# Kernel optimization log

Hardware: AMD Instinct MI355X
Metric: run time of the kernel (lower is better)

The kernel has to match this reference:

```python
import jax, jax.numpy as jnp
import numpy as np

INPUT_SIZE = 128
HIDDEN_SIZE = 128
OUTPUT_SIZE = 67  # hardcoded in the original module
SEQ_LEN = 512
BATCH = 2048


def setup_inputs() -> dict:
    key = jax.random.key(0)
    ks = jax.random.split(key, 7)
    x = jax.random.normal(ks[0], (INPUT_SIZE, SEQ_LEN, BATCH), dtype=jnp.float32)
    hidden = jax.random.normal(ks[1], (HIDDEN_SIZE, BATCH), dtype=jnp.float32)
    # bernoulli(0.5) mask applied column-wise to the initial hidden state
    drop_mask = jax.random.bernoulli(ks[2], 0.5, (HIDDEN_SIZE, BATCH)).astype(jnp.float32)
    # small init scale so tanh does not saturate
    Wi2h = jax.random.normal(ks[3], (HIDDEN_SIZE, INPUT_SIZE + HIDDEN_SIZE), dtype=jnp.float32) * 0.05
    bi2h = jax.random.normal(ks[4], (HIDDEN_SIZE,), dtype=jnp.float32) * 0.05
    Wi2o = jax.random.normal(ks[5], (OUTPUT_SIZE, HIDDEN_SIZE), dtype=jnp.float32) * 0.05
    bi2o = jax.random.normal(ks[6], (OUTPUT_SIZE,), dtype=jnp.float32) * 0.05
    return {"x": x, "hidden": hidden, "drop_mask": drop_mask,
            "Wi2h": Wi2h, "bi2h": bi2h, "Wi2o": Wi2o, "bi2o": bi2o}


def reference(x, hidden, drop_mask, Wi2h, bi2h, Wi2o, bi2o):
    # x: [input_size, seq_len, batch]; hidden: [hidden_size, batch]
    h0 = hidden * drop_mask  # per-column bernoulli dropout on initial state
    xs = jnp.transpose(x, (1, 0, 2))  # [seq, input_size, batch]

    def step(h, x_t):
        # combined = cat([x_t, h], dim=0).T -> [batch, input+hidden]
        combined = jnp.concatenate([x_t, h], axis=0).T
        h_new = jnp.tanh(combined @ Wi2h.T + bi2h)        # [batch, hidden]
        out = jax.nn.relu(h_new @ Wi2o.T + bi2o)          # [batch, output]
        return h_new.T, out.T                             # carry [hidden, batch], y [output, batch]

    _, ys = jax.lax.scan(step, h0, xs)  # ys: [seq, output, batch]
    Y = jnp.transpose(ys, (1, 0, 2))    # [output, seq, batch]
    return Y
```

## Files before the change

### kernel.cpp

```cpp
#include <hip/hip_runtime.h>
#include <hip/hip_bf16.h>
#include <stdint.h>

#define IN_SZ 128
#define HID 128
#define OUT_SZ 67
#define SEQ 512
#define BATCH 2048
#define BT 8
#define NTHR 512
#define SB (SEQ * BATCH)

typedef __attribute__((ext_vector_type(4))) float f32x4;
typedef __attribute__((ext_vector_type(8))) short s16x8;
typedef __attribute__((ext_vector_type(8))) __bf16 bf16x8;

static __device__ __forceinline__ unsigned short f2bf(float f) {
  union { float f; uint32_t u; } c; c.f = f;
  uint32_t u = c.u;
  uint32_t r = u + 0x7FFFu + ((u >> 16) & 1u);
  return (unsigned short)(r >> 16);
}
static __device__ __forceinline__ uint32_t pk2bf(float lo, float hi) {
  __hip_bfloat162 h2 = __float22bfloat162_rn(float2{lo, hi});
  union { __hip_bfloat162 h; uint32_t u; } c; c.h = h2;
  return c.u;
}
static __device__ __forceinline__ float fast_tanh(float x) {
  float e = __builtin_amdgcn_exp2f(x * 2.885390081777927f);
  float r = __builtin_amdgcn_rcpf(e + 1.f);
  return __builtin_fmaf(-2.f, r, 1.f);
}
static __device__ __forceinline__ void mfma16(f32x4& c, s16x8 a, s16x8 b) {
  c = __builtin_amdgcn_mfma_f32_16x16x32_bf16(
        __builtin_bit_cast(bf16x8, a), __builtin_bit_cast(bf16x8, b), c, 0, 0, 0);
}
#define KOFF(g, j) (4 * (g) + ((j) & 3) + (((j) >> 2) << 4))

static __device__ __forceinline__ void frag_barrier() {
  asm volatile("s_waitcnt lgkmcnt(0)");
  __builtin_amdgcn_s_barrier();
}

__global__ __launch_bounds__(NTHR, 1) void rnn_kernel(
    const float* __restrict__ x, const float* __restrict__ hidden,
    const float* __restrict__ mask, const float* __restrict__ Wi2h,
    const float* __restrict__ bi2h, const float* __restrict__ Wi2o,
    const float* __restrict__ bi2o, float* __restrict__ Y) {

  __shared__ s16x8 sF[2][8][64];

  const int tid = threadIdx.x;
  const int wave = tid >> 6;
  const int lane = tid & 63;
  const int g = lane >> 4;
  const int n16 = lane & 15;
  const int bid = ((blockIdx.x & 7) << 5) | (blockIdx.x >> 3);
  const int b0 = bid * BT;

  s16x8 W[8];
#pragma unroll
  for (int kt = 0; kt < 8; ++kt) {
    const float* wr = Wi2h + (size_t)(16 * wave + n16) * (IN_SZ + HID);
    s16x8 w8;
#pragma unroll
    for (int j = 0; j < 8; ++j)
      w8[j] = (short)f2bf(wr[32 * kt + KOFF(g, j)]);
    W[kt] = w8;
  }

  const bool hasO = (wave < 5);
  s16x8 wO[4];
#pragma unroll
  for (int kk = 0; kk < 4; ++kk) {
    s16x8 a;
#pragma unroll
    for (int j = 0; j < 8; ++j) {
      int m = 16 * wave + n16;
      a[j] = (short)((hasO && m < OUT_SZ)
                     ? f2bf(Wi2o[(size_t)m * HID + 32 * kk + KOFF(g, j)]) : 0);
    }
    wO[kk] = a;
  }

  f32x4 bhv, bov;
#pragma unroll
  for (int r = 0; r < 4; ++r) {
    bhv[r] = bi2h[16 * wave + 4 * g + r];
    int m = 16 * wave + 4 * g + r;
    bov[r] = (hasO && m < OUT_SZ) ? bi2o[m] : 0.f;
  }

  const int lc = tid & 7;
  const int lrb = tid >> 3;
  const int R0 = 2 * lrb;
  const int skk = R0 >> 5;
  const int r5 = R0 & 31;
  const int sg = (r5 < 16) ? (r5 >> 2) : ((r5 - 16) >> 2);
  const int sq = ((r5 & 2) >> 1) + ((r5 < 16) ? 0 : 2);
  const int slane = (sg << 4) | lc;
  const char* const xB = (const char*)x;
  uint32_t xrb[2];
#pragma unroll
  for (int i = 0; i < 2; ++i)
    xrb[i] = ((uint32_t)(R0 + i) * (uint32_t)SB + (uint32_t)(b0 + lc)) * 4u;

  {
    float v0 = *(const float*)(xB + xrb[0]);
    float v1 = *(const float*)(xB + xrb[1]);
    ((uint32_t*)&sF[0][skk][slane])[sq] = pk2bf(v0, v1);
    uint32_t h0o = (uint32_t)R0 * (uint32_t)BATCH + (uint32_t)(b0 + lc);
    uint32_t h1o = (uint32_t)(R0 + 1) * (uint32_t)BATCH + (uint32_t)(b0 + lc);
    float hv0 = hidden[(size_t)h0o] * mask[(size_t)h0o];
    float hv1 = hidden[(size_t)h1o] * mask[(size_t)h1o];
    ((uint32_t*)&sF[0][4 + skk][slane])[sq] = pk2bf(hv0, hv1);
  }
  float xq0[2], xq1[2], xq2[2], xq3[2];
#pragma unroll
  for (int i = 0; i < 2; ++i) {
    xq0[i] = *(const float*)(xB + xrb[i] + 1u * BATCH * 4u);
    xq1[i] = *(const float*)(xB + xrb[i] + 2u * BATCH * 4u);
    xq2[i] = *(const float*)(xB + xrb[i] + 3u * BATCH * 4u);
    xq3[i] = *(const float*)(xB + xrb[i] + 4u * BATCH * 4u);
  }
  frag_barrier();

  const uint32_t ybase = (uint32_t)(16 * wave + 4 * g) * (uint32_t)SB + (uint32_t)(b0 + n16);
  uint32_t* const hdst0 = (uint32_t*)&sF[0][4 + (wave >> 1)][lane] + (wave & 1) * 2;
  uint32_t* const hdst1 = (uint32_t*)&sF[1][4 + (wave >> 1)][lane] + (wave & 1) * 2;

#define STEP(T, P, XQ)                                                          \
  {                                                                             \
    const int t = (T);                                                          \
    const int pn = (P) ^ 1;                                                     \
                  \
    ((uint32_t*)&sF[pn][skk][slane])[sq] = pk2bf(XQ[0], XQ[1]);                 \
                                          \
    {                                                                           \
      const uint32_t tn = (uint32_t)((t + 5 > 511) ? 511 : t + 5) * (BATCH * 4u); \
      XQ[0] = *(const float*)(xB + xrb[0] + tn);                                \
      XQ[1] = *(const float*)(xB + xrb[1] + tn);                                \
    }                                                                           \
                                        \
    s16x8 X0 = sF[P][0][lane], X1 = sF[P][1][lane];                             \
    s16x8 X2 = sF[P][2][lane], X3 = sF[P][3][lane];                             \
    s16x8 H0 = sF[P][4][lane], H1 = sF[P][5][lane];                             \
    s16x8 H2 = sF[P][6][lane], H3 = sF[P][7][lane];                             \
                         \
    f32x4 a = bhv, a2 = {0.f, 0.f, 0.f, 0.f};                                   \
    mfma16(a, W[4], H0);  mfma16(a2, W[5], H1);                                 \
    mfma16(a, W[6], H2);  mfma16(a2, W[7], H3);                                 \
    mfma16(a, W[0], X0);  mfma16(a2, W[1], X1);                                 \
    mfma16(a, W[2], X2);  mfma16(a2, W[3], X3);                                 \
                                                   \
    if (hasO && t > 0) {                                                        \
      const uint32_t ty = (uint32_t)(t - 1) * (uint32_t)BATCH;                  \
      f32x4 ao = bov;                                                           \
      mfma16(ao, wO[0], H0); mfma16(ao, wO[1], H1);                             \
      mfma16(ao, wO[2], H2); mfma16(ao, wO[3], H3);                             \
      if (n16 < BT) {                                                           \
        _Pragma("unroll")                                                       \
        for (int r = 0; r < 4; ++r)                                             \
          if (16 * wave + 4 * g + r < OUT_SZ)                                   \
            Y[(size_t)(ybase + (uint32_t)r * SB + ty)] = fmaxf(ao[r], 0.f);     \
      }                                                                         \
    }                                                                           \
                      \
    {                                                                           \
      f32x4 s0 = a + a2;                                                        \
      uint32_t hp[2];                                                           \
      hp[0] = pk2bf(fast_tanh(s0[0]), fast_tanh(s0[1]));                        \
      hp[1] = pk2bf(fast_tanh(s0[2]), fast_tanh(s0[3]));                        \
      uint32_t* hd = pn ? hdst1 : hdst0;                                        \
      *(uint64_t*)hd = *(uint64_t*)hp;                                          \
    }                                                                           \
    frag_barrier();                                                             \
  }

  for (int t4 = 0; t4 < SEQ; t4 += 4) {
    STEP(t4 + 0, 0, xq0);
    STEP(t4 + 1, 1, xq1);
    STEP(t4 + 2, 0, xq2);
    STEP(t4 + 3, 1, xq3);
  }
#undef STEP

  if (hasO) {
    s16x8 H0 = sF[0][4][lane], H1 = sF[0][5][lane];
    s16x8 H2 = sF[0][6][lane], H3 = sF[0][7][lane];
    const uint32_t ty = 511u * (uint32_t)BATCH;
    f32x4 ao = bov;
    mfma16(ao, wO[0], H0); mfma16(ao, wO[1], H1);
    mfma16(ao, wO[2], H2); mfma16(ao, wO[3], H3);
    if (n16 < BT) {
#pragma unroll
      for (int r = 0; r < 4; ++r)
        if (16 * wave + 4 * g + r < OUT_SZ)
          Y[(size_t)(ybase + (uint32_t)r * SB + ty)] = fmaxf(ao[r], 0.f);
    }
  }
}

extern "C" void kernel_launch(void* const* d_in, const int* in_sizes, int n_in,
                              void* d_out, int out_size, void* d_ws, size_t ws_size,
                              hipStream_t stream) {
  const float* x      = (const float*)d_in[0];
  const float* hidden = (const float*)d_in[1];
  const float* mask   = (const float*)d_in[2];
  const float* Wi2h   = (const float*)d_in[3];
  const float* bi2h   = (const float*)d_in[4];
  const float* Wi2o   = (const float*)d_in[5];
  const float* bi2o   = (const float*)d_in[6];
  float* Y = (float*)d_out;
  (void)in_sizes; (void)n_in; (void)out_size; (void)d_ws; (void)ws_size;
  rnn_kernel<<<dim3(BATCH / BT), dim3(NTHR), 0, stream>>>(
      x, hidden, mask, Wi2h, bi2h, Wi2o, bi2o, Y);
}
```

Baseline: 530.5 us.

## Stage x via global_load_lds ring and move output MFMA off critical path

Replaces register-held prefetch of x with direct global-to-LDS DMA loads into a 4-slot ring buffer, so each step reads its x slice from LDS after a vmcnt wait. The tanh/h-write now happens before the barrier and the output projection with its Y stores is moved after the barrier, taking it off the recurrent critical path. The x-part MFMAs go into separate accumulators to shorten dependency chains. The risk is that the vmcnt(4) counting mixes with the Y stores' vmem counts, and ring-slot reuse timing may stall or race.

```diff
diff --git a/kernel.cpp b/kernel.cpp
--- a/kernel.cpp
+++ b/kernel.cpp
@@ -15,6 +15,9 @@
 typedef __attribute__((ext_vector_type(8))) short s16x8;
 typedef __attribute__((ext_vector_type(8))) __bf16 bf16x8;
 
+typedef const uint32_t __attribute__((address_space(1))) gu32_t;
+typedef uint32_t __attribute__((address_space(3))) su32_t;
+
 static __device__ __forceinline__ unsigned short f2bf(float f) {
   union { float f; uint32_t u; } c; c.f = f;
   uint32_t u = c.u;
@@ -41,6 +44,10 @@
   asm volatile("s_waitcnt lgkmcnt(0)");
   __builtin_amdgcn_s_barrier();
 }
+static __device__ __forceinline__ void dma4(const float* src, float* dst) {
+  __builtin_amdgcn_global_load_lds((gu32_t*)(const void*)src,
+                                   (su32_t*)(void*)dst, 4, 0, 0);
+}
 
 __global__ __launch_bounds__(NTHR, 1) void rnn_kernel(
     const float* __restrict__ x, const float* __restrict__ hidden,
@@ -49,6 +56,7 @@
     const float* __restrict__ bi2o, float* __restrict__ Y) {
 
   __shared__ s16x8 sF[2][8][64];
+  __shared__ float sX[4][1024];
 
   const int tid = threadIdx.x;
   const int wave = tid >> 6;
@@ -90,6 +98,9 @@
     int m = 16 * wave + 4 * g + r;
     bov[r] = (hasO && m < OUT_SZ) ? bi2o[m] : 0.f;
   }
+
+  const float* dma0 = x + (size_t)(16 * wave + (lane >> 3)) * SB + b0 + (lane & 7);
+  const float* dma1 = dma0 + (size_t)8 * SB;
 
   const int lc = tid & 7;
   const int lrb = tid >> 3;
@@ -99,15 +110,11 @@
   const int sg = (r5 < 16) ? (r5 >> 2) : ((r5 - 16) >> 2);
   const int sq = ((r5 & 2) >> 1) + ((r5 < 16) ? 0 : 2);
   const int slane = (sg << 4) | lc;
-  const char* const xB = (const char*)x;
-  uint32_t xrb[2];
-#pragma unroll
-  for (int i = 0; i < 2; ++i)
-    xrb[i] = ((uint32_t)(R0 + i) * (uint32_t)SB + (uint32_t)(b0 + lc)) * 4u;
+  const int e0 = R0 * 8 + lc;
 
   {
-    float v0 = *(const float*)(xB + xrb[0]);
-    float v1 = *(const float*)(xB + xrb[1]);
+    float v0 = x[(size_t)R0 * SB + b0 + lc];
+    float v1 = x[(size_t)(R0 + 1) * SB + b0 + lc];
     ((uint32_t*)&sF[0][skk][slane])[sq] = pk2bf(v0, v1);
     uint32_t h0o = (uint32_t)R0 * (uint32_t)BATCH + (uint32_t)(b0 + lc);
     uint32_t h1o = (uint32_t)(R0 + 1) * (uint32_t)BATCH + (uint32_t)(b0 + lc);
@@ -115,44 +122,59 @@
     float hv1 = hidden[(size_t)h1o] * mask[(size_t)h1o];
     ((uint32_t*)&sF[0][4 + skk][slane])[sq] = pk2bf(hv0, hv1);
   }
-  float xq0[2], xq1[2], xq2[2], xq3[2];
-#pragma unroll
-  for (int i = 0; i < 2; ++i) {
-    xq0[i] = *(const float*)(xB + xrb[i] + 1u * BATCH * 4u);
-    xq1[i] = *(const float*)(xB + xrb[i] + 2u * BATCH * 4u);
-    xq2[i] = *(const float*)(xB + xrb[i] + 3u * BATCH * 4u);
-    xq3[i] = *(const float*)(xB + xrb[i] + 4u * BATCH * 4u);
-  }
+
+#define STAGE(T, D)                                                             \
+  {                                                                             \
+    const uint32_t tp = ((T) > 511 ? 511u : (uint32_t)(T)) * (uint32_t)BATCH;   \
+    dma4(dma0 + tp, &sX[D][128 * wave]);                                        \
+    dma4(dma1 + tp, &sX[D][128 * wave + 64]);                                   \
+  }
+
+  STAGE(1, 1)
+  STAGE(2, 2)
+  STAGE(3, 3)
   frag_barrier();
 
   const uint32_t ybase = (uint32_t)(16 * wave + 4 * g) * (uint32_t)SB + (uint32_t)(b0 + n16);
   uint32_t* const hdst0 = (uint32_t*)&sF[0][4 + (wave >> 1)][lane] + (wave & 1) * 2;
   uint32_t* const hdst1 = (uint32_t*)&sF[1][4 + (wave >> 1)][lane] + (wave & 1) * 2;
 
-#define STEP(T, P, XQ)                                                          \
+#define STEP(T, P, D)                                                           \
   {                                                                             \
     const int t = (T);                                                          \
     const int pn = (P) ^ 1;                                                     \
-                  \
-    ((uint32_t*)&sF[pn][skk][slane])[sq] = pk2bf(XQ[0], XQ[1]);                 \
-                                          \
-    {                                                                           \
-      const uint32_t tn = (uint32_t)((t + 5 > 511) ? 511 : t + 5) * (BATCH * 4u); \
-      XQ[0] = *(const float*)(xB + xrb[0] + tn);                                \
-      XQ[1] = *(const float*)(xB + xrb[1] + tn);                                \
-    }                                                                           \
                                         \
     s16x8 X0 = sF[P][0][lane], X1 = sF[P][1][lane];                             \
     s16x8 X2 = sF[P][2][lane], X3 = sF[P][3][lane];                             \
     s16x8 H0 = sF[P][4][lane], H1 = sF[P][5][lane];                             \
     s16x8 H2 = sF[P][6][lane], H3 = sF[P][7][lane];                             \
-                         \
+                                   \
     f32x4 a = bhv, a2 = {0.f, 0.f, 0.f, 0.f};                                   \
-    mfma16(a, W[4], H0);  mfma16(a2, W[5], H1);                                 \
-    mfma16(a, W[6], H2);  mfma16(a2, W[7], H3);                                 \
-    mfma16(a, W[0], X0);  mfma16(a2, W[1], X1);                                 \
-    mfma16(a, W[2], X2);  mfma16(a2, W[3], X3);                                 \
-                                                   \
+    f32x4 ax = {0.f, 0.f, 0.f, 0.f}, ax2 = {0.f, 0.f, 0.f, 0.f};                \
+    mfma16(a, W[4], H0);   mfma16(a2, W[5], H1);                                \
+    mfma16(ax, W[0], X0);  mfma16(ax2, W[1], X1);                               \
+    mfma16(a, W[6], H2);   mfma16(a2, W[7], H3);                                \
+    mfma16(ax, W[2], X2);  mfma16(ax2, W[3], X3);                               \
+       \
+    {                                                                           \
+      f32x4 s0 = (a + a2) + (ax + ax2);                                         \
+      uint32_t hp[2];                                                           \
+      hp[0] = pk2bf(fast_tanh(s0[0]), fast_tanh(s0[1]));                        \
+      hp[1] = pk2bf(fast_tanh(s0[2]), fast_tanh(s0[3]));                        \
+      uint32_t* hd = pn ? hdst1 : hdst0;                                        \
+      *(uint64_t*)hd = *(uint64_t*)hp;                                          \
+    }                                                                           \
+                   \
+    asm volatile("s_waitcnt vmcnt(4)");                                         \
+    __builtin_amdgcn_sched_barrier(0);                                          \
+    {                                                                           \
+      float v0 = sX[D][e0];                                                     \
+      float v1 = sX[D][e0 + 8];                                                 \
+      ((uint32_t*)&sF[pn][skk][slane])[sq] = pk2bf(v0, v1);                     \
+    }                                                                           \
+                                                         \
+    frag_barrier();                                                             \
+              \
     if (hasO && t > 0) {                                                        \
       const uint32_t ty = (uint32_t)(t - 1) * (uint32_t)BATCH;                  \
       f32x4 ao = bov;                                                           \
@@ -165,25 +187,17 @@
             Y[(size_t)(ybase + (uint32_t)r * SB + ty)] = fmaxf(ao[r], 0.f);     \
       }                                                                         \
     }                                                                           \
-                      \
-    {                                                                           \
-      f32x4 s0 = a + a2;                                                        \
-      uint32_t hp[2];                                                           \
-      hp[0] = pk2bf(fast_tanh(s0[0]), fast_tanh(s0[1]));                        \
-      hp[1] = pk2bf(fast_tanh(s0[2]), fast_tanh(s0[3]));                        \
-      uint32_t* hd = pn ? hdst1 : hdst0;                                        \
-      *(uint64_t*)hd = *(uint64_t*)hp;                                          \
-    }                                                                           \
-    frag_barrier();                                                             \
+    STAGE(t + 4, (T) & 3)                                                       \
   }
 
   for (int t4 = 0; t4 < SEQ; t4 += 4) {
-    STEP(t4 + 0, 0, xq0);
-    STEP(t4 + 1, 1, xq1);
-    STEP(t4 + 2, 0, xq2);
-    STEP(t4 + 3, 1, xq3);
+    STEP(t4 + 0, 0, 1);
+    STEP(t4 + 1, 1, 2);
+    STEP(t4 + 2, 0, 3);
+    STEP(t4 + 3, 1, 0);
   }
 #undef STEP
+#undef STAGE
 
   if (hasO) {
     s16x8 H0 = sF[0][4][lane], H1 = sF[0][5][lane];
```

Result: slower. 673.9 us (+27.0%).

## Precompute next step's input projection off the recurrent critical path

Applied to the files above, without the earlier changes.

Splits the shared fragment buffer into separate hidden (double-buffered) and input (triple-buffered) arrays. The x-part MFMAs for step t+1 are issued during step t, so each step's dependent chain after the barrier is only the four hidden-state MFMAs plus tanh. The tanh and hidden write are also moved ahead of the output projection and Y stores. Sched barriers are added around the frag barrier to pin instruction ordering, which costs more registers and a 6-way unrolled loop with a tail.

```diff
diff --git a/kernel.cpp b/kernel.cpp
--- a/kernel.cpp
+++ b/kernel.cpp
@@ -38,8 +38,10 @@
 #define KOFF(g, j) (4 * (g) + ((j) & 3) + (((j) >> 2) << 4))
 
 static __device__ __forceinline__ void frag_barrier() {
+  __builtin_amdgcn_sched_barrier(0);
   asm volatile("s_waitcnt lgkmcnt(0)");
   __builtin_amdgcn_s_barrier();
+  __builtin_amdgcn_sched_barrier(0);
 }
 
 __global__ __launch_bounds__(NTHR, 1) void rnn_kernel(
@@ -48,7 +50,8 @@
     const float* __restrict__ bi2h, const float* __restrict__ Wi2o,
     const float* __restrict__ bi2o, float* __restrict__ Y) {
 
-  __shared__ s16x8 sF[2][8][64];
+  __shared__ s16x8 sH[2][4][64];
+  __shared__ s16x8 sX[3][4][64];
 
   const int tid = threadIdx.x;
   const int wave = tid >> 6;
@@ -100,94 +103,105 @@
   const int sq = ((r5 & 2) >> 1) + ((r5 < 16) ? 0 : 2);
   const int slane = (sg << 4) | lc;
   const char* const xB = (const char*)x;
-  uint32_t xrb[2];
-#pragma unroll
-  for (int i = 0; i < 2; ++i)
-    xrb[i] = ((uint32_t)(R0 + i) * (uint32_t)SB + (uint32_t)(b0 + lc)) * 4u;
+  const uint32_t xrb0 = ((uint32_t)R0 * (uint32_t)SB + (uint32_t)(b0 + lc)) * 4u;
+  const uint32_t xrb1 = ((uint32_t)(R0 + 1) * (uint32_t)SB + (uint32_t)(b0 + lc)) * 4u;
 
   {
-    float v0 = *(const float*)(xB + xrb[0]);
-    float v1 = *(const float*)(xB + xrb[1]);
-    ((uint32_t*)&sF[0][skk][slane])[sq] = pk2bf(v0, v1);
+    float v0 = *(const float*)(xB + xrb0);
+    float v1 = *(const float*)(xB + xrb1);
+    ((uint32_t*)&sX[0][skk][slane])[sq] = pk2bf(v0, v1);
+    float w0 = *(const float*)(xB + xrb0 + BATCH * 4u);
+    float w1 = *(const float*)(xB + xrb1 + BATCH * 4u);
+    ((uint32_t*)&sX[1][skk][slane])[sq] = pk2bf(w0, w1);
     uint32_t h0o = (uint32_t)R0 * (uint32_t)BATCH + (uint32_t)(b0 + lc);
     uint32_t h1o = (uint32_t)(R0 + 1) * (uint32_t)BATCH + (uint32_t)(b0 + lc);
     float hv0 = hidden[(size_t)h0o] * mask[(size_t)h0o];
     float hv1 = hidden[(size_t)h1o] * mask[(size_t)h1o];
-    ((uint32_t*)&sF[0][4 + skk][slane])[sq] = pk2bf(hv0, hv1);
-  }
-  float xq0[2], xq1[2], xq2[2], xq3[2];
-#pragma unroll
-  for (int i = 0; i < 2; ++i) {
-    xq0[i] = *(const float*)(xB + xrb[i] + 1u * BATCH * 4u);
-    xq1[i] = *(const float*)(xB + xrb[i] + 2u * BATCH * 4u);
-    xq2[i] = *(const float*)(xB + xrb[i] + 3u * BATCH * 4u);
-    xq3[i] = *(const float*)(xB + xrb[i] + 4u * BATCH * 4u);
-  }
+    ((uint32_t*)&sH[0][skk][slane])[sq] = pk2bf(hv0, hv1);
+  }
+  float xqA[2], xqB[2];
+  xqA[0] = *(const float*)(xB + xrb0 + 2u * BATCH * 4u);
+  xqA[1] = *(const float*)(xB + xrb1 + 2u * BATCH * 4u);
+  xqB[0] = *(const float*)(xB + xrb0 + 3u * BATCH * 4u);
+  xqB[1] = *(const float*)(xB + xrb1 + 3u * BATCH * 4u);
   frag_barrier();
 
   const uint32_t ybase = (uint32_t)(16 * wave + 4 * g) * (uint32_t)SB + (uint32_t)(b0 + n16);
-  uint32_t* const hdst0 = (uint32_t*)&sF[0][4 + (wave >> 1)][lane] + (wave & 1) * 2;
-  uint32_t* const hdst1 = (uint32_t*)&sF[1][4 + (wave >> 1)][lane] + (wave & 1) * 2;
-
-#define STEP(T, P, XQ)                                                          \
-  {                                                                             \
-    const int t = (T);                                                          \
-    const int pn = (P) ^ 1;                                                     \
-                  \
-    ((uint32_t*)&sF[pn][skk][slane])[sq] = pk2bf(XQ[0], XQ[1]);                 \
+  uint32_t* const hdst0 = (uint32_t*)&sH[0][wave >> 1][lane] + (wave & 1) * 2;
+  uint32_t* const hdst1 = (uint32_t*)&sH[1][wave >> 1][lane] + (wave & 1) * 2;
+
+  f32x4 axA = bhv, axA2 = {0.f, 0.f, 0.f, 0.f};
+  f32x4 axB, axB2;
+  {
+    s16x8 X0 = sX[0][0][lane], X1 = sX[0][1][lane];
+    s16x8 X2 = sX[0][2][lane], X3 = sX[0][3][lane];
+    mfma16(axA, W[0], X0);  mfma16(axA2, W[1], X1);
+    mfma16(axA, W[2], X2);  mfma16(axA2, W[3], X3);
+  }
+
+#define ITER(K, SR, SW, HPAR, XQ, AXI, AXI2, AXO, AXO2)                        \
+  {                                                                            \
+    const int t = t6 + (K);                                                    \
+    s16x8 H0 = sH[HPAR][0][lane], H1 = sH[HPAR][1][lane];                      \
+    s16x8 H2 = sH[HPAR][2][lane], H3 = sH[HPAR][3][lane];                      \
+    s16x8 Xn0 = sX[SR][0][lane], Xn1 = sX[SR][1][lane];                        \
+    s16x8 Xn2 = sX[SR][2][lane], Xn3 = sX[SR][3][lane];                        \
                                           \
-    {                                                                           \
-      const uint32_t tn = (uint32_t)((t + 5 > 511) ? 511 : t + 5) * (BATCH * 4u); \
-      XQ[0] = *(const float*)(xB + xrb[0] + tn);                                \
-      XQ[1] = *(const float*)(xB + xrb[1] + tn);                                \
-    }                                                                           \
-                                        \
-    s16x8 X0 = sF[P][0][lane], X1 = sF[P][1][lane];                             \
-    s16x8 X2 = sF[P][2][lane], X3 = sF[P][3][lane];                             \
-    s16x8 H0 = sF[P][4][lane], H1 = sF[P][5][lane];                             \
-    s16x8 H2 = sF[P][6][lane], H3 = sF[P][7][lane];                             \
-                         \
-    f32x4 a = bhv, a2 = {0.f, 0.f, 0.f, 0.f};                                   \
-    mfma16(a, W[4], H0);  mfma16(a2, W[5], H1);                                 \
-    mfma16(a, W[6], H2);  mfma16(a2, W[7], H3);                                 \
-    mfma16(a, W[0], X0);  mfma16(a2, W[1], X1);                                 \
-    mfma16(a, W[2], X2);  mfma16(a2, W[3], X3);                                 \
-                                                   \
-    if (hasO && t > 0) {                                                        \
-      const uint32_t ty = (uint32_t)(t - 1) * (uint32_t)BATCH;                  \
-      f32x4 ao = bov;                                                           \
-      mfma16(ao, wO[0], H0); mfma16(ao, wO[1], H1);                             \
-      mfma16(ao, wO[2], H2); mfma16(ao, wO[3], H3);                             \
-      if (n16 < BT) {                                                           \
-        _Pragma("unroll")                                                       \
-        for (int r = 0; r < 4; ++r)                                             \
-          if (16 * wave + 4 * g + r < OUT_SZ)                                   \
-            Y[(size_t)(ybase + (uint32_t)r * SB + ty)] = fmaxf(ao[r], 0.f);     \
-      }                                                                         \
-    }                                                                           \
-                      \
-    {                                                                           \
-      f32x4 s0 = a + a2;                                                        \
-      uint32_t hp[2];                                                           \
-      hp[0] = pk2bf(fast_tanh(s0[0]), fast_tanh(s0[1]));                        \
-      hp[1] = pk2bf(fast_tanh(s0[2]), fast_tanh(s0[3]));                        \
-      uint32_t* hd = pn ? hdst1 : hdst0;                                        \
-      *(uint64_t*)hd = *(uint64_t*)hp;                                          \
-    }                                                                           \
-    frag_barrier();                                                             \
-  }
-
-  for (int t4 = 0; t4 < SEQ; t4 += 4) {
-    STEP(t4 + 0, 0, xq0);
-    STEP(t4 + 1, 1, xq1);
-    STEP(t4 + 2, 0, xq2);
-    STEP(t4 + 3, 1, xq3);
-  }
-#undef STEP
+    mfma16(AXI, W[4], H0);   mfma16(AXI2, W[5], H1);                           \
+    mfma16(AXI, W[6], H2);   mfma16(AXI2, W[7], H3);                           \
+                                              \
+    AXO = bhv; AXO2 = (f32x4){0.f, 0.f, 0.f, 0.f};                             \
+    mfma16(AXO, W[0], Xn0);  mfma16(AXO2, W[1], Xn1);                          \
+    mfma16(AXO, W[2], Xn2);  mfma16(AXO2, W[3], Xn3);                          \
+       \
+    {                                                                          \
+      f32x4 s0 = AXI + AXI2;                                                   \
+      uint32_t hpq[2];                                                         \
+      hpq[0] = pk2bf(fast_tanh(s0[0]), fast_tanh(s0[1]));                      \
+      hpq[1] = pk2bf(fast_tanh(s0[2]), fast_tanh(s0[3]));                      \
+      *(uint64_t*)((HPAR) ? hdst0 : hdst1) = *(uint64_t*)hpq;                  \
+    }                                                                          \
+                                     \
+    if (hasO && t > 0) {                                                       \
+      const uint32_t ty = (uint32_t)(t - 1) * (uint32_t)BATCH;                 \
+      f32x4 ao = bov;                                                          \
+      mfma16(ao, wO[0], H0); mfma16(ao, wO[1], H1);                            \
+      mfma16(ao, wO[2], H2); mfma16(ao, wO[3], H3);                            \
+      if (n16 < BT) {                                                          \
+        _Pragma("unroll")                                                      \
+        for (int r = 0; r < 4; ++r)                                            \
+          if (16 * wave + 4 * g + r < OUT_SZ)                                  \
+            Y[(size_t)(ybase + (uint32_t)r * SB + ty)] = fmaxf(ao[r], 0.f);    \
+      }                                                                        \
+    }                                                                          \
+                                 \
+    ((uint32_t*)&sX[SW][skk][slane])[sq] = pk2bf(XQ[0], XQ[1]);                \
+    {                                                                          \
+      const uint32_t tn = (uint32_t)((t + 4 > 511) ? 511 : t + 4) * (BATCH * 4u); \
+      XQ[0] = *(const float*)(xB + xrb0 + tn);                                 \
+      XQ[1] = *(const float*)(xB + xrb1 + tn);                                 \
+    }                                                                          \
+    frag_barrier();                                                            \
+  }
+
+  for (int t6 = 0; t6 < 510; t6 += 6) {
+    ITER(0, 1, 2, 0, xqA, axA, axA2, axB, axB2)
+    ITER(1, 2, 0, 1, xqB, axB, axB2, axA, axA2)
+    ITER(2, 0, 1, 0, xqA, axA, axA2, axB, axB2)
+    ITER(3, 1, 2, 1, xqB, axB, axB2, axA, axA2)
+    ITER(4, 2, 0, 0, xqA, axA, axA2, axB, axB2)
+    ITER(5, 0, 1, 1, xqB, axB, axB2, axA, axA2)
+  }
+  {
+    const int t6 = 510;
+    ITER(0, 1, 2, 0, xqA, axA, axA2, axB, axB2)
+    ITER(1, 2, 0, 1, xqB, axB, axB2, axA, axA2)
+  }
+#undef ITER
 
   if (hasO) {
-    s16x8 H0 = sF[0][4][lane], H1 = sF[0][5][lane];
-    s16x8 H2 = sF[0][6][lane], H3 = sF[0][7][lane];
+    s16x8 H0 = sH[0][0][lane], H1 = sH[0][1][lane];
+    s16x8 H2 = sH[0][2][lane], H3 = sH[0][3][lane];
     const uint32_t ty = 511u * (uint32_t)BATCH;
     f32x4 ao = bov;
     mfma16(ao, wO[0], H0); mfma16(ao, wO[1], H1);
```

Measured after the change: 594.6 us. 1.12x slower.

## Split output projection onto dedicated waves, off the recurrent critical path

Applied to the files above, without the earlier changes.

Raises the block from 8 to 10 waves. The first 8 waves compute only the recurrent hidden update, now using four independent MFMA accumulators to shorten the dependency chain. The 2 extra waves hold the Wi2o fragments and compute and store the ReLU outputs for the previous step in lockstep with the barriers. The aim is to take the output MFMAs and global stores out of the serial per-step path, at the cost of more threads per block and barrier participants, plus sched_barrier fences around each barrier.

```diff
diff --git a/kernel.cpp b/kernel.cpp
--- a/kernel.cpp
+++ b/kernel.cpp
@@ -8,7 +8,7 @@
 #define SEQ 512
 #define BATCH 2048
 #define BT 8
-#define NTHR 512
+#define NTHR 640
 #define SB (SEQ * BATCH)
 
 typedef __attribute__((ext_vector_type(4))) float f32x4;
@@ -38,8 +38,10 @@
 #define KOFF(g, j) (4 * (g) + ((j) & 3) + (((j) >> 2) << 4))
 
 static __device__ __forceinline__ void frag_barrier() {
+  __builtin_amdgcn_sched_barrier(0);
   asm volatile("s_waitcnt lgkmcnt(0)");
   __builtin_amdgcn_s_barrier();
+  __builtin_amdgcn_sched_barrier(0);
 }
 
 __global__ __launch_bounds__(NTHR, 1) void rnn_kernel(
@@ -58,145 +60,172 @@
   const int bid = ((blockIdx.x & 7) << 5) | (blockIdx.x >> 3);
   const int b0 = bid * BT;
 
-  s16x8 W[8];
-#pragma unroll
-  for (int kt = 0; kt < 8; ++kt) {
-    const float* wr = Wi2h + (size_t)(16 * wave + n16) * (IN_SZ + HID);
-    s16x8 w8;
-#pragma unroll
-    for (int j = 0; j < 8; ++j)
-      w8[j] = (short)f2bf(wr[32 * kt + KOFF(g, j)]);
-    W[kt] = w8;
-  }
-
-  const bool hasO = (wave < 5);
-  s16x8 wO[4];
-#pragma unroll
-  for (int kk = 0; kk < 4; ++kk) {
-    s16x8 a;
-#pragma unroll
-    for (int j = 0; j < 8; ++j) {
-      int m = 16 * wave + n16;
-      a[j] = (short)((hasO && m < OUT_SZ)
-                     ? f2bf(Wi2o[(size_t)m * HID + 32 * kk + KOFF(g, j)]) : 0);
-    }
-    wO[kk] = a;
-  }
-
-  f32x4 bhv, bov;
-#pragma unroll
-  for (int r = 0; r < 4; ++r) {
-    bhv[r] = bi2h[16 * wave + 4 * g + r];
-    int m = 16 * wave + 4 * g + r;
-    bov[r] = (hasO && m < OUT_SZ) ? bi2o[m] : 0.f;
-  }
-
-  const int lc = tid & 7;
-  const int lrb = tid >> 3;
-  const int R0 = 2 * lrb;
-  const int skk = R0 >> 5;
-  const int r5 = R0 & 31;
-  const int sg = (r5 < 16) ? (r5 >> 2) : ((r5 - 16) >> 2);
-  const int sq = ((r5 & 2) >> 1) + ((r5 < 16) ? 0 : 2);
-  const int slane = (sg << 4) | lc;
-  const char* const xB = (const char*)x;
-  uint32_t xrb[2];
-#pragma unroll
-  for (int i = 0; i < 2; ++i)
-    xrb[i] = ((uint32_t)(R0 + i) * (uint32_t)SB + (uint32_t)(b0 + lc)) * 4u;
-
-  {
-    float v0 = *(const float*)(xB + xrb[0]);
-    float v1 = *(const float*)(xB + xrb[1]);
-    ((uint32_t*)&sF[0][skk][slane])[sq] = pk2bf(v0, v1);
-    uint32_t h0o = (uint32_t)R0 * (uint32_t)BATCH + (uint32_t)(b0 + lc);
-    uint32_t h1o = (uint32_t)(R0 + 1) * (uint32_t)BATCH + (uint32_t)(b0 + lc);
-    float hv0 = hidden[(size_t)h0o] * mask[(size_t)h0o];
-    float hv1 = hidden[(size_t)h1o] * mask[(size_t)h1o];
-    ((uint32_t*)&sF[0][4 + skk][slane])[sq] = pk2bf(hv0, hv1);
-  }
-  float xq0[2], xq1[2], xq2[2], xq3[2];
-#pragma unroll
-  for (int i = 0; i < 2; ++i) {
-    xq0[i] = *(const float*)(xB + xrb[i] + 1u * BATCH * 4u);
-    xq1[i] = *(const float*)(xB + xrb[i] + 2u * BATCH * 4u);
-    xq2[i] = *(const float*)(xB + xrb[i] + 3u * BATCH * 4u);
-    xq3[i] = *(const float*)(xB + xrb[i] + 4u * BATCH * 4u);
-  }
-  frag_barrier();
-
-  const uint32_t ybase = (uint32_t)(16 * wave + 4 * g) * (uint32_t)SB + (uint32_t)(b0 + n16);
-  uint32_t* const hdst0 = (uint32_t*)&sF[0][4 + (wave >> 1)][lane] + (wave & 1) * 2;
-  uint32_t* const hdst1 = (uint32_t*)&sF[1][4 + (wave >> 1)][lane] + (wave & 1) * 2;
-
-#define STEP(T, P, XQ)                                                          \
+  if (wave < 8) {
+    s16x8 W[8];
+#pragma unroll
+    for (int kt = 0; kt < 8; ++kt) {
+      const float* wr = Wi2h + (size_t)(16 * wave + n16) * (IN_SZ + HID);
+      s16x8 w8;
+#pragma unroll
+      for (int j = 0; j < 8; ++j)
+        w8[j] = (short)f2bf(wr[32 * kt + KOFF(g, j)]);
+      W[kt] = w8;
+    }
+    f32x4 bhv;
+#pragma unroll
+    for (int r = 0; r < 4; ++r) bhv[r] = bi2h[16 * wave + 4 * g + r];
+
+    const int lc = tid & 7;
+    const int lrb = tid >> 3;
+    const int R0 = 2 * lrb;
+    const int skk = R0 >> 5;
+    const int r5 = R0 & 31;
+    const int sg = (r5 < 16) ? (r5 >> 2) : ((r5 - 16) >> 2);
+    const int sq = ((r5 & 2) >> 1) + ((r5 < 16) ? 0 : 2);
+    const int slane = (sg << 4) | lc;
+    const char* const xB = (const char*)x;
+    const uint32_t xrb0 = ((uint32_t)R0 * (uint32_t)SB + (uint32_t)(b0 + lc)) * 4u;
+    const uint32_t xrb1 = ((uint32_t)(R0 + 1) * (uint32_t)SB + (uint32_t)(b0 + lc)) * 4u;
+
+    {
+      float v0 = *(const float*)(xB + xrb0);
+      float v1 = *(const float*)(xB + xrb1);
+      ((uint32_t*)&sF[0][skk][slane])[sq] = pk2bf(v0, v1);
+      uint32_t h0o = (uint32_t)R0 * (uint32_t)BATCH + (uint32_t)(b0 + lc);
+      uint32_t h1o = (uint32_t)(R0 + 1) * (uint32_t)BATCH + (uint32_t)(b0 + lc);
+      float hv0 = hidden[(size_t)h0o] * mask[(size_t)h0o];
+      float hv1 = hidden[(size_t)h1o] * mask[(size_t)h1o];
+      ((uint32_t*)&sF[0][4 + skk][slane])[sq] = pk2bf(hv0, hv1);
+    }
+    float xq0[2], xq1[2], xq2[2], xq3[2];
+    xq0[0] = *(const float*)(xB + xrb0 + 1u * BATCH * 4u);
+    xq0[1] = *(const float*)(xB + xrb1 + 1u * BATCH * 4u);
+    xq1[0] = *(const float*)(xB + xrb0 + 2u * BATCH * 4u);
+    xq1[1] = *(const float*)(xB + xrb1 + 2u * BATCH * 4u);
+    xq2[0] = *(const float*)(xB + xrb0 + 3u * BATCH * 4u);
+    xq2[1] = *(const float*)(xB + xrb1 + 3u * BATCH * 4u);
+    xq3[0] = *(const float*)(xB + xrb0 + 4u * BATCH * 4u);
+    xq3[1] = *(const float*)(xB + xrb1 + 4u * BATCH * 4u);
+    frag_barrier();
+
+    uint32_t* const hdst0 = (uint32_t*)&sF[0][4 + (wave >> 1)][lane] + (wave & 1) * 2;
+    uint32_t* const hdst1 = (uint32_t*)&sF[1][4 + (wave >> 1)][lane] + (wave & 1) * 2;
+
+#define STEPC(T, P, XQ)                                                         \
   {                                                                             \
     const int t = (T);                                                          \
     const int pn = (P) ^ 1;                                                     \
-                  \
+               \
     ((uint32_t*)&sF[pn][skk][slane])[sq] = pk2bf(XQ[0], XQ[1]);                 \
-                                          \
     {                                                                           \
       const uint32_t tn = (uint32_t)((t + 5 > 511) ? 511 : t + 5) * (BATCH * 4u); \
-      XQ[0] = *(const float*)(xB + xrb[0] + tn);                                \
-      XQ[1] = *(const float*)(xB + xrb[1] + tn);                                \
+      XQ[0] = *(const float*)(xB + xrb0 + tn);                                  \
+      XQ[1] = *(const float*)(xB + xrb1 + tn);                                  \
     }                                                                           \
-                                        \
+                                           \
     s16x8 X0 = sF[P][0][lane], X1 = sF[P][1][lane];                             \
     s16x8 X2 = sF[P][2][lane], X3 = sF[P][3][lane];                             \
     s16x8 H0 = sF[P][4][lane], H1 = sF[P][5][lane];                             \
     s16x8 H2 = sF[P][6][lane], H3 = sF[P][7][lane];                             \
-                         \
+                                      \
     f32x4 a = bhv, a2 = {0.f, 0.f, 0.f, 0.f};                                   \
-    mfma16(a, W[4], H0);  mfma16(a2, W[5], H1);                                 \
-    mfma16(a, W[6], H2);  mfma16(a2, W[7], H3);                                 \
-    mfma16(a, W[0], X0);  mfma16(a2, W[1], X1);                                 \
-    mfma16(a, W[2], X2);  mfma16(a2, W[3], X3);                                 \
-                                                   \
-    if (hasO && t > 0) {                                                        \
-      const uint32_t ty = (uint32_t)(t - 1) * (uint32_t)BATCH;                  \
-      f32x4 ao = bov;                                                           \
-      mfma16(ao, wO[0], H0); mfma16(ao, wO[1], H1);                             \
-      mfma16(ao, wO[2], H2); mfma16(ao, wO[3], H3);                             \
-      if (n16 < BT) {                                                           \
-        _Pragma("unroll")                                                       \
-        for (int r = 0; r < 4; ++r)                                             \
-          if (16 * wave + 4 * g + r < OUT_SZ)                                   \
-            Y[(size_t)(ybase + (uint32_t)r * SB + ty)] = fmaxf(ao[r], 0.f);     \
-      }                                                                         \
-    }                                                                           \
-                      \
+    f32x4 ax = {0.f, 0.f, 0.f, 0.f}, ax2 = {0.f, 0.f, 0.f, 0.f};                \
+    mfma16(a, W[4], H0);   mfma16(a2, W[5], H1);                                \
+    mfma16(ax, W[0], X0);  mfma16(ax2, W[1], X1);                               \
+    mfma16(a, W[6], H2);   mfma16(a2, W[7], H3);                                \
+    mfma16(ax, W[2], X2);  mfma16(ax2, W[3], X3);                               \
+        \
     {                                                                           \
-      f32x4 s0 = a + a2;                                                        \
+      f32x4 s0 = (a + a2) + (ax + ax2);                                         \
       uint32_t hp[2];                                                           \
       hp[0] = pk2bf(fast_tanh(s0[0]), fast_tanh(s0[1]));                        \
       hp[1] = pk2bf(fast_tanh(s0[2]), fast_tanh(s0[3]));                        \
-      uint32_t* hd = pn ? hdst1 : hdst0;                                        \
-      *(uint64_t*)hd = *(uint64_t*)hp;                                          \
+      *(uint64_t*)(pn ? hdst1 : hdst0) = *(uint64_t*)hp;                        \
     }                                                                           \
     frag_barrier();                                                             \
   }
 
-  for (int t4 = 0; t4 < SEQ; t4 += 4) {
-    STEP(t4 + 0, 0, xq0);
-    STEP(t4 + 1, 1, xq1);
-    STEP(t4 + 2, 0, xq2);
-    STEP(t4 + 3, 1, xq3);
-  }
-#undef STEP
-
-  if (hasO) {
-    s16x8 H0 = sF[0][4][lane], H1 = sF[0][5][lane];
-    s16x8 H2 = sF[0][6][lane], H3 = sF[0][7][lane];
-    const uint32_t ty = 511u * (uint32_t)BATCH;
-    f32x4 ao = bov;
-    mfma16(ao, wO[0], H0); mfma16(ao, wO[1], H1);
-    mfma16(ao, wO[2], H2); mfma16(ao, wO[3], H3);
-    if (n16 < BT) {
-#pragma unroll
-      for (int r = 0; r < 4; ++r)
-        if (16 * wave + 4 * g + r < OUT_SZ)
-          Y[(size_t)(ybase + (uint32_t)r * SB + ty)] = fmaxf(ao[r], 0.f);
+    for (int t4 = 0; t4 < SEQ; t4 += 4) {
+      STEPC(t4 + 0, 0, xq0)
+      STEPC(t4 + 1, 1, xq1)
+      STEPC(t4 + 2, 0, xq2)
+      STEPC(t4 + 3, 1, xq3)
+    }
+#undef STEPC
+
+  } else {
+    const int ow = wave - 8;
+    s16x8 wO[3][4];
+    f32x4 bov[3];
+    uint32_t ybase[3];
+    bool tvalid[3];
+#pragma unroll
+    for (int ot = 0; ot < 3; ++ot) {
+      const int tk = 3 * ow + ot;
+      tvalid[ot] = (tk < 5);
+#pragma unroll
+      for (int kk = 0; kk < 4; ++kk) {
+        s16x8 a;
+#pragma unroll
+        for (int j = 0; j < 8; ++j) {
+          int m = 16 * tk + n16;
+          a[j] = (short)((tvalid[ot] && m < OUT_SZ)
+                         ? f2bf(Wi2o[(size_t)m * HID + 32 * kk + KOFF(g, j)]) : 0);
+        }
+        wO[ot][kk] = a;
+      }
+#pragma unroll
+      for (int r = 0; r < 4; ++r) {
+        int m = 16 * tk + 4 * g + r;
+        bov[ot][r] = (tvalid[ot] && m < OUT_SZ) ? bi2o[m] : 0.f;
+      }
+      ybase[ot] = (uint32_t)(16 * tk + 4 * g) * (uint32_t)SB + (uint32_t)(b0 + n16);
+    }
+
+    frag_barrier();
+    frag_barrier();
+
+    for (int t = 1; t < SEQ; ++t) {
+      const int P = t & 1;
+      s16x8 H0 = sF[P][4][lane], H1 = sF[P][5][lane];
+      s16x8 H2 = sF[P][6][lane], H3 = sF[P][7][lane];
+      const uint32_t ty = (uint32_t)(t - 1) * (uint32_t)BATCH;
+#pragma unroll
+      for (int ot = 0; ot < 3; ++ot) {
+        if (tvalid[ot]) {
+          const int tk = 3 * ow + ot;
+          f32x4 ao = bov[ot];
+          mfma16(ao, wO[ot][0], H0); mfma16(ao, wO[ot][1], H1);
+          mfma16(ao, wO[ot][2], H2); mfma16(ao, wO[ot][3], H3);
+          if (n16 < BT) {
+#pragma unroll
+            for (int r = 0; r < 4; ++r)
+              if (16 * tk + 4 * g + r < OUT_SZ)
+                Y[(size_t)(ybase[ot] + (uint32_t)r * SB + ty)] = fmaxf(ao[r], 0.f);
+          }
+        }
+      }
+      frag_barrier();
+    }
+    {
+      s16x8 H0 = sF[0][4][lane], H1 = sF[0][5][lane];
+      s16x8 H2 = sF[0][6][lane], H3 = sF[0][7][lane];
+      const uint32_t ty = 511u * (uint32_t)BATCH;
+#pragma unroll
+      for (int ot = 0; ot < 3; ++ot) {
+        if (tvalid[ot]) {
+          const int tk = 3 * ow + ot;
+          f32x4 ao = bov[ot];
+          mfma16(ao, wO[ot][0], H0); mfma16(ao, wO[ot][1], H1);
+          mfma16(ao, wO[ot][2], H2); mfma16(ao, wO[ot][3], H3);
+          if (n16 < BT) {
+#pragma unroll
+            for (int r = 0; r < 4; ++r)
+              if (16 * tk + 4 * g + r < OUT_SZ)
+                Y[(size_t)(ybase[ot] + (uint32_t)r * SB + ty)] = fmaxf(ao[r], 0.f);
+          }
+        }
+      }
     }
   }
 }
```

Result: faster. 518.4 us (-2.3%).
